# Performance work log

Hardware: AMD Instinct MI355X
Metric: run time of the kernel (lower is better)

The kernel has to match this reference:

```python
import jax, jax.numpy as jnp
import numpy as np

B, IC, H, W = 32, 128, 112, 112
OC, K, STRIDE, PAD = 256, 3, 2, 1


def setup_inputs() -> dict:
    key = jax.random.key(0)
    kx, kw = jax.random.split(key)
    x = jax.random.normal(kx, (B, IC, H, W), dtype=jnp.float32)
    weight = jax.random.normal(kw, (OC, IC, K, K), dtype=jnp.float32) * 0.01
    bias = jnp.zeros((OC,), dtype=jnp.float32)
    return {"x": x, "weight": weight, "bias": bias}


def reference(x, weight, bias):
    # Equivalent of the nested-loop conv: standard cross-correlation,
    # stride=2, zero padding=1, NCHW / OIHW layouts.
    out = jax.lax.conv_general_dilated(
        x, weight,
        window_strides=(STRIDE, STRIDE),
        padding=[(PAD, PAD), (PAD, PAD)],
        dimension_numbers=("NCHW", "OIHW", "NCHW"),
    )
    return out + bias[None, :, None, None]
```

## Files before the change

kernel.cpp:

```cpp
#include <hip/hip_runtime.h>
#include <hip/hip_bf16.h>
#include <type_traits>


#define B_    32
#define IC_   128
#define H_    112
#define W_    112
#define HW_   (H_ * W_)
#define OC_   256
#define NPIX  (B_ * 56 * 56)
#define NTILE (NPIX / 64)
#define WT2_BYTES ((size_t)36 * 16384)

typedef __attribute__((ext_vector_type(8))) short bf16x8;
typedef __attribute__((ext_vector_type(8))) float f32x8;
typedef __attribute__((ext_vector_type(4))) float f32x4;

struct WReg { uint4 a, b, c, d; };

static __device__ __forceinline__ unsigned f2bf_u(float f) {
  union { float f; unsigned u; } v; v.f = f;
  return (v.u + 0x7FFF + ((v.u >> 16) & 1)) >> 16;
}

static __device__ __forceinline__ unsigned pk_bf16(float a, float b) {
  union { __hip_bfloat162 h; unsigned u; } c;
  c.h = __float22bfloat162_rn(float2{a, b});
  return c.u;
}

__global__ __launch_bounds__(256) void wtrans2_kernel(
    const float* __restrict__ w, unsigned short* __restrict__ wt2) {
  const int t  = blockIdx.x * 256 + threadIdx.x;
  const int oc = t >> 7;
  const int ic = t & 127;
  const int icc = ic >> 5, q = (ic >> 3) & 3, e = ic & 7;
  const float* ws = w + (size_t)t * 9;
#pragma unroll
  for (int tap = 0; tap < 9; ++tap) {
    const int step = tap * 4 + icc;
    wt2[((size_t)(step * 4 + q) * 256 + oc) * 8 + e] =
        (unsigned short)f2bf_u(ws[tap]);
  }
}

__global__ __launch_bounds__(256, 2) void conv_fused_kernel(
    const float* __restrict__ x, const unsigned short* __restrict__ wt2,
    const float* __restrict__ bias, float* __restrict__ out) {
  __shared__ unsigned short Wl[4][8192];
  __shared__ unsigned short Xl[4][2048];

  const int tid = threadIdx.x, wav = tid >> 6, lane = tid & 63;

  const int bid = blockIdx.x;
  const int pt  = (bid & 7) * (NTILE / 8) + (bid >> 3);
  const int p0  = pt * 64;
  const int b   = p0 / 3136;
  const int q0  = p0 - b * 3136;

  const int pixq = q0 + lane;
  const int oh = pixq / 56, ow = pixq - oh * 56;
  const int ih0 = 2 * oh - 1, iw0 = 2 * ow - 1;
  const int boff = ih0 * W_ + iw0;
  const float* xpl = x + (size_t)b * IC_ * HW_;

  unsigned mtap = 0;
#pragma unroll
  for (int kh = 0; kh < 3; ++kh)
#pragma unroll
    for (int kw = 0; kw < 3; ++kw)
      if (ih0 + kh >= 0 && iw0 + kw >= 0) mtap |= 1u << (kh * 3 + kw);

  const int l15 = lane & 15, lg = lane >> 4;
  const char* wsrc = reinterpret_cast<const char*>(wt2) + wav * 1024 + lane * 16;

  auto loadX = [&](int s) -> f32x8 {
    const int tap = s >> 2, icc = s & 3;
    const int kh = tap / 3, kw = tap - kh * 3;
    const bool m = (mtap >> tap) & 1;
    const int o  = boff + kh * W_ + kw + (icc * 32 + wav * 8) * HW_;
    const int ob = m ? o : (icc * 32 + wav * 8) * HW_;
    f32x8 v;
#pragma unroll
    for (int k = 0; k < 8; ++k) {
      const float t = xpl[ob + k * HW_];
      v[k] = m ? t : 0.f;
    }
    return v;
  };
  auto loadW = [&](int s) -> WReg {
    const char* src = wsrc + (size_t)s * 16384;
    WReg r;
    r.a = *reinterpret_cast<const uint4*>(src);
    r.b = *reinterpret_cast<const uint4*>(src + 4096);
    r.c = *reinterpret_cast<const uint4*>(src + 8192);
    r.d = *reinterpret_cast<const uint4*>(src + 12288);
    return r;
  };
  auto writeX = [&](const f32x8& v, int buf) {
    uint4 p;
    p.x = pk_bf16(v[0], v[1]);
    p.y = pk_bf16(v[2], v[3]);
    p.z = pk_bf16(v[4], v[5]);
    p.w = pk_bf16(v[6], v[7]);
    *reinterpret_cast<uint4*>(
        reinterpret_cast<char*>(&Xl[buf][0]) + wav * 1024 + lane * 16) = p;
  };
  auto writeW = [&](const WReg& r, int buf) {
    char* dst = reinterpret_cast<char*>(&Wl[buf][0]) + wav * 1024 + lane * 16;
    *reinterpret_cast<uint4*>(dst)         = r.a;
    *reinterpret_cast<uint4*>(dst + 4096)  = r.b;
    *reinterpret_cast<uint4*>(dst + 8192)  = r.c;
    *reinterpret_cast<uint4*>(dst + 12288) = r.d;
  };

  f32x4 acc[4][4] = {};

  auto compute = [&](int buf) {
    bf16x8 af[4], bx[4];
    const unsigned short* wb  = &Wl[buf][0] + lg * 2048;
    const unsigned short* xb2 = &Xl[buf][0] + lg * 512;
#pragma unroll
    for (int mi = 0; mi < 4; ++mi)
      af[mi] = *reinterpret_cast<const bf16x8*>(
          wb + (wav * 64 + mi * 16 + l15) * 8);
#pragma unroll
    for (int ni = 0; ni < 4; ++ni)
      bx[ni] = *reinterpret_cast<const bf16x8*>(xb2 + (ni * 16 + l15) * 8);
#pragma unroll
    for (int mi = 0; mi < 4; ++mi)
#pragma unroll
      for (int ni = 0; ni < 4; ++ni)
        acc[mi][ni] = __builtin_amdgcn_mfma_f32_16x16x32_bf16(
            af[mi], bx[ni], acc[mi][ni], 0, 0, 0);
  };

  f32x8 xa, xb_, xc;
  WReg  wa, wb_, wc;

  xa = loadX(0); wa = loadW(0);
  xb_ = loadX(1); wb_ = loadW(1);
  xc = loadX(2); wc = loadW(2);
  writeX(xa, 0); writeW(wa, 0);
  asm volatile("s_waitcnt lgkmcnt(0)" ::: "memory");
  __builtin_amdgcn_sched_barrier(0);
  __builtin_amdgcn_s_barrier();
  __builtin_amdgcn_sched_barrier(0);

  auto phase = [&](auto KC, int sb) {
    constexpr int K = decltype(KC)::value;
    const int s = sb + K;
    f32x8& xn = (K % 3 == 0) ? xa : (K % 3 == 1) ? xb_ : xc;
    WReg&  wn = (K % 3 == 0) ? wa : (K % 3 == 1) ? wb_ : wc;
    f32x8& xm = ((K + 1) % 3 == 0) ? xa : ((K + 1) % 3 == 1) ? xb_ : xc;
    WReg&  wm = ((K + 1) % 3 == 0) ? wa : ((K + 1) % 3 == 1) ? wb_ : wc;
    if (s + 3 < 36) { xn = loadX(s + 3); wn = loadW(s + 3); }
    if (s + 1 < 36) { writeX(xm, (K + 1) & 3); writeW(wm, (K + 1) & 3); }
    asm volatile("s_waitcnt lgkmcnt(0)" ::: "memory");
    __builtin_amdgcn_sched_barrier(0);
    __builtin_amdgcn_s_barrier();
    __builtin_amdgcn_sched_barrier(0);
    compute(K & 3);
  };

#define PH(K) phase(std::integral_constant<int, K>{}, sb)
  for (int sb = 0; sb < 36; sb += 12) {
    PH(0); PH(1); PH(2); PH(3); PH(4); PH(5);
    PH(6); PH(7); PH(8); PH(9); PH(10); PH(11);
  }
#undef PH

#pragma unroll
  for (int mi = 0; mi < 4; ++mi) {
#pragma unroll
    for (int j = 0; j < 4; ++j) {
      const int oc = wav * 64 + mi * 16 + lg * 4 + j;
      const float bv = bias[oc];
#pragma unroll
      for (int ni = 0; ni < 4; ++ni) {
        const int qp = q0 + ni * 16 + l15;
        out[((size_t)b * OC_ + oc) * 3136 + qp] = acc[mi][ni][j] + bv;
      }
    }
  }
}

__global__ __launch_bounds__(256) void conv2d_f32_kernel(
    const float* __restrict__ x, const float* __restrict__ w,
    const float* __restrict__ bias, float* __restrict__ out) {
  __shared__ float wlds[IC_ * 9][8];
  const int b   = blockIdx.z;
  const int oc0 = blockIdx.y * 8;
  const float* wsrc = w + (size_t)oc0 * (IC_ * 9);
  for (int i = threadIdx.x; i < IC_ * 9 * 8; i += 256) {
    const int j = i / (IC_ * 9);
    const int t = i - j * (IC_ * 9);
    wlds[t][j] = wsrc[(size_t)j * (IC_ * 9) + t];
  }
  __syncthreads();
  const int p  = blockIdx.x * 256 + threadIdx.x;
  const int ow = p % 56;
  const int oh = p / 56;
  const bool pv = (oh < 56);
  const int ih0 = 2 * oh - 1;
  const int iw0 = 2 * ow - 1;
  const float* xb = x + (size_t)b * IC_ * HW_ + (ptrdiff_t)ih0 * W_ + iw0;
  float acc[8];
#pragma unroll
  for (int j = 0; j < 8; ++j) acc[j] = 0.f;
  for (int ic = 0; ic < IC_; ++ic) {
    const float* xc = xb + (size_t)ic * HW_;
#pragma unroll
    for (int kh = 0; kh < 3; ++kh) {
      const bool hv = pv && ((ih0 + kh) >= 0);
#pragma unroll
      for (int kw = 0; kw < 3; ++kw) {
        const bool v = hv && ((iw0 + kw) >= 0);
        const float xv = v ? xc[kh * W_ + kw] : 0.f;
        const int t = ic * 9 + kh * 3 + kw;
        const float4 w0 = *reinterpret_cast<const float4*>(&wlds[t][0]);
        const float4 w1 = *reinterpret_cast<const float4*>(&wlds[t][4]);
        acc[0] = fmaf(xv, w0.x, acc[0]); acc[1] = fmaf(xv, w0.y, acc[1]);
        acc[2] = fmaf(xv, w0.z, acc[2]); acc[3] = fmaf(xv, w0.w, acc[3]);
        acc[4] = fmaf(xv, w1.x, acc[4]); acc[5] = fmaf(xv, w1.y, acc[5]);
        acc[6] = fmaf(xv, w1.z, acc[6]); acc[7] = fmaf(xv, w1.w, acc[7]);
      }
    }
  }
  if (pv) {
#pragma unroll
    for (int j = 0; j < 8; ++j)
      out[(((size_t)(b * OC_ + oc0 + j)) * 56 + oh) * 56 + ow] =
          acc[j] + bias[oc0 + j];
  }
}

extern "C" void kernel_launch(void* const* d_in, const int* in_sizes, int n_in,
                              void* d_out, int out_size, void* d_ws, size_t ws_size,
                              hipStream_t stream) {
  const float* x    = (const float*)d_in[0];
  const float* w    = (const float*)d_in[1];
  const float* bias = (const float*)d_in[2];
  float* out        = (float*)d_out;

  if (ws_size >= WT2_BYTES) {
    unsigned short* wt2 = (unsigned short*)d_ws;
    wtrans2_kernel<<<128, 256, 0, stream>>>(w, wt2);
    conv_fused_kernel<<<NTILE, 256, 0, stream>>>(x, wt2, bias, out);
  } else {
    conv2d_f32_kernel<<<dim3(13, OC_ / 8, B_), 256, 0, stream>>>(x, w, bias, out);
  }
}
```

Measured before the change: 169.2 us.

## Load weight MFMA fragments directly from global into registers, drop weight LDS staging

Removes the shared-memory staging buffer for weights. Each wave now loads its own MFMA A-fragments straight from the pre-transposed global weight buffer into registers, double-buffered one step ahead. This frees 64KB of LDS per block and drops the LDS write/read traffic for weights, so launch bounds are raised to allow 3 blocks per CU. In exchange, weight loads now have only one step of prefetch distance instead of three, and the four waves no longer share a single staged copy. This relies on L2/L1 to absorb the duplicated reads and risks exposing global-load latency before each compute.

```diff
diff --git a/kernel.cpp b/kernel.cpp
--- a/kernel.cpp
+++ b/kernel.cpp
@@ -17,7 +17,7 @@
 typedef __attribute__((ext_vector_type(8))) float f32x8;
 typedef __attribute__((ext_vector_type(4))) float f32x4;
 
-struct WReg { uint4 a, b, c, d; };
+struct AF { bf16x8 m[4]; };
 
 static __device__ __forceinline__ unsigned f2bf_u(float f) {
   union { float f; unsigned u; } v; v.f = f;
@@ -45,10 +45,9 @@
   }
 }
 
-__global__ __launch_bounds__(256, 2) void conv_fused_kernel(
+__global__ __launch_bounds__(256, 3) void conv_fused_kernel(
     const float* __restrict__ x, const unsigned short* __restrict__ wt2,
     const float* __restrict__ bias, float* __restrict__ out) {
-  __shared__ unsigned short Wl[4][8192];
   __shared__ unsigned short Xl[4][2048];
 
   const int tid = threadIdx.x, wav = tid >> 6, lane = tid & 63;
@@ -73,7 +72,6 @@
       if (ih0 + kh >= 0 && iw0 + kw >= 0) mtap |= 1u << (kh * 3 + kw);
 
   const int l15 = lane & 15, lg = lane >> 4;
-  const char* wsrc = reinterpret_cast<const char*>(wt2) + wav * 1024 + lane * 16;
 
   auto loadX = [&](int s) -> f32x8 {
     const int tap = s >> 2, icc = s & 3;
@@ -89,13 +87,13 @@
     }
     return v;
   };
-  auto loadW = [&](int s) -> WReg {
-    const char* src = wsrc + (size_t)s * 16384;
-    WReg r;
-    r.a = *reinterpret_cast<const uint4*>(src);
-    r.b = *reinterpret_cast<const uint4*>(src + 4096);
-    r.c = *reinterpret_cast<const uint4*>(src + 8192);
-    r.d = *reinterpret_cast<const uint4*>(src + 12288);
+  auto loadAF = [&](int s) -> AF {
+    const unsigned short* src =
+        wt2 + (size_t)s * 8192 + lg * 2048 + (wav * 64 + l15) * 8;
+    AF r;
+#pragma unroll
+    for (int mi = 0; mi < 4; ++mi)
+      r.m[mi] = *reinterpret_cast<const bf16x8*>(src + mi * 128);
     return r;
   };
   auto writeX = [&](const f32x8& v, int buf) {
@@ -107,24 +105,12 @@
     *reinterpret_cast<uint4*>(
         reinterpret_cast<char*>(&Xl[buf][0]) + wav * 1024 + lane * 16) = p;
   };
-  auto writeW = [&](const WReg& r, int buf) {
-    char* dst = reinterpret_cast<char*>(&Wl[buf][0]) + wav * 1024 + lane * 16;
-    *reinterpret_cast<uint4*>(dst)         = r.a;
-    *reinterpret_cast<uint4*>(dst + 4096)  = r.b;
-    *reinterpret_cast<uint4*>(dst + 8192)  = r.c;
-    *reinterpret_cast<uint4*>(dst + 12288) = r.d;
-  };
 
   f32x4 acc[4][4] = {};
 
-  auto compute = [&](int buf) {
-    bf16x8 af[4], bx[4];
-    const unsigned short* wb  = &Wl[buf][0] + lg * 2048;
+  auto compute = [&](int buf, const AF& af) {
+    bf16x8 bx[4];
     const unsigned short* xb2 = &Xl[buf][0] + lg * 512;
-#pragma unroll
-    for (int mi = 0; mi < 4; ++mi)
-      af[mi] = *reinterpret_cast<const bf16x8*>(
-          wb + (wav * 64 + mi * 16 + l15) * 8);
 #pragma unroll
     for (int ni = 0; ni < 4; ++ni)
       bx[ni] = *reinterpret_cast<const bf16x8*>(xb2 + (ni * 16 + l15) * 8);
@@ -133,43 +119,45 @@
 #pragma unroll
       for (int ni = 0; ni < 4; ++ni)
         acc[mi][ni] = __builtin_amdgcn_mfma_f32_16x16x32_bf16(
-            af[mi], bx[ni], acc[mi][ni], 0, 0, 0);
+            af.m[mi], bx[ni], acc[mi][ni], 0, 0, 0);
   };
 
   f32x8 xa, xb_, xc;
-  WReg  wa, wb_, wc;
-
-  xa = loadX(0); wa = loadW(0);
-  xb_ = loadX(1); wb_ = loadW(1);
-  xc = loadX(2); wc = loadW(2);
-  writeX(xa, 0); writeW(wa, 0);
+  AF afE, afO;
+
+  afE = loadAF(0);
+  xa = loadX(0);
+  xb_ = loadX(1);
+  xc = loadX(2);
+  writeX(xa, 0);
   asm volatile("s_waitcnt lgkmcnt(0)" ::: "memory");
   __builtin_amdgcn_sched_barrier(0);
   __builtin_amdgcn_s_barrier();
   __builtin_amdgcn_sched_barrier(0);
 
-  auto phase = [&](auto KC, int sb) {
+  auto phase = [&](auto KC, int sb, AF& afCur, AF& afNxt) {
     constexpr int K = decltype(KC)::value;
     const int s = sb + K;
+    if (s + 1 < 36) afNxt = loadAF(s + 1);
     f32x8& xn = (K % 3 == 0) ? xa : (K % 3 == 1) ? xb_ : xc;
-    WReg&  wn = (K % 3 == 0) ? wa : (K % 3 == 1) ? wb_ : wc;
     f32x8& xm = ((K + 1) % 3 == 0) ? xa : ((K + 1) % 3 == 1) ? xb_ : xc;
-    WReg&  wm = ((K + 1) % 3 == 0) ? wa : ((K + 1) % 3 == 1) ? wb_ : wc;
-    if (s + 3 < 36) { xn = loadX(s + 3); wn = loadW(s + 3); }
-    if (s + 1 < 36) { writeX(xm, (K + 1) & 3); writeW(wm, (K + 1) & 3); }
+    if (s + 3 < 36) xn = loadX(s + 3);
+    if (s + 1 < 36) writeX(xm, (K + 1) & 3);
     asm volatile("s_waitcnt lgkmcnt(0)" ::: "memory");
     __builtin_amdgcn_sched_barrier(0);
     __builtin_amdgcn_s_barrier();
     __builtin_amdgcn_sched_barrier(0);
-    compute(K & 3);
-  };
-
-#define PH(K) phase(std::integral_constant<int, K>{}, sb)
+    compute(K & 3, afCur);
+  };
+
+#define PHE(K) phase(std::integral_constant<int, K>{}, sb, afE, afO)
+#define PHO(K) phase(std::integral_constant<int, K>{}, sb, afO, afE)
   for (int sb = 0; sb < 36; sb += 12) {
-    PH(0); PH(1); PH(2); PH(3); PH(4); PH(5);
-    PH(6); PH(7); PH(8); PH(9); PH(10); PH(11);
-  }
-#undef PH
+    PHE(0); PHO(1); PHE(2); PHO(3); PHE(4); PHO(5);
+    PHE(6); PHO(7); PHE(8); PHO(9); PHE(10); PHO(11);
+  }
+#undef PHE
+#undef PHO
 
 #pragma unroll
   for (int mi = 0; mi < 4; ++mi) {
```

New measurement: 223.4 us. +32.0%, slower.
